# Kernel tuning notes

Measured on AMD Instinct MI355X. Metric: run time of the kernel, lower is better.

The kernel has to match this reference:

```python
import jax, jax.numpy as jnp
import numpy as np

BONE_NUM = 16
THRESH = 0.7


def masked_l2(out, tar, mask):
    # out, tar: [B, C, H, W]; mask: [B, H, W]
    diff_norm = jnp.linalg.norm(out - tar, axis=1)          # [B, H, W]
    masked = jnp.where(mask > THRESH, diff_norm, 0.0)
    B = out.shape[0]
    flat_m = masked.reshape(B, -1)
    flat_d = diff_norm.reshape(B, -1)
    cnt = jnp.sum(flat_m != 0, axis=1)                       # device-side nonzero count
    per_sample = jnp.where(
        cnt > 0,
        flat_m.sum(axis=1) / jnp.maximum(cnt, 1).astype(flat_m.dtype),
        flat_d.mean(axis=1),
    )
    return per_sample.mean()


def pose_nocs_loss(pred_joint_map, pred_joint_score, out_mask, tar_joints):
    # pred_joint_map: [B, bn*3, H, W]; pred_joint_score: [B, bn, H, W]
    # out_mask: [B, H, W]; tar_joints: [B, bn, 3]
    B, _, H, W = pred_joint_map.shape
    bn = BONE_NUM
    jm = pred_joint_map.reshape(B, bn, 3, H, W) * out_mask[:, None, None]
    score = jax.nn.sigmoid(pred_joint_score) * out_mask[:, None]        # [B, bn, H, W]
    denom = score.reshape(B, bn, -1).sum(axis=2)[:, :, None, None] + 1e-5
    score_map = score / denom
    jm = jax.lax.stop_gradient(jm) * score_map[:, :, None]              # [B, bn, 3, H, W]
    pred_joint = jm.reshape(B, bn, 3, -1).sum(axis=3)                   # [B, bn, 3]
    loss = jnp.linalg.norm(pred_joint - tar_joints, axis=2).sum()
    return loss / (B * bn)


def setup_inputs() -> dict:
    key = jax.random.key(0)
    k1, k2, k3 = jax.random.split(key, 3)
    B, H, W = 4, 256, 256
    bn = BONE_NUM
    output = jax.random.normal(k1, (B, 4 + bn * 8 + 2, H, W), dtype=jnp.float32)
    tar_maps = jax.random.uniform(k2, (B, 4 + bn * 6 + 1, H, W), dtype=jnp.float32)
    tar_pose = jax.random.normal(k3, (B, bn, 6), dtype=jnp.float32)
    return {"output": output, "tar_maps": tar_maps, "tar_pose": tar_pose}


def reference(output, tar_maps, tar_pose):
    bn = BONE_NUM
    B = output.shape[0]

    # --- slice predictions ---
    pred_nocs = output[:, 0:3]
    mask_logits = output[:, 3]                                # sigmoid applied below
    pred_loc_map = jax.nn.sigmoid(output[:, 4:4 + bn * 3])
    pred_rot_map = jax.nn.sigmoid(output[:, 4 + bn * 3:4 + bn * 6])
    pred_skin_seg = output[:, 4 + bn * 6:4 + bn * 7 + 2]       # [B, bn+2, H, W]
    pred_joint_score = output[:, 4 + bn * 7 + 2:4 + bn * 8 + 2]  # [B, bn, H, W]

    # --- slice targets ---
    target_nocs = tar_maps[:, 0:3]
    target_mask = tar_maps[:, 3]
    tar_loc_map = jax.nn.sigmoid(tar_maps[:, 4:4 + bn * 3])
    tar_rot_map = jax.nn.sigmoid(tar_maps[:, 4 + bn * 3:4 + bn * 6])
    tar_skin_seg = tar_maps[:, 4 + bn * 6].astype(jnp.int32)   # [B, H, W]
    tar_loc = jax.nn.sigmoid(tar_pose[:, :, 0:3])
    tar_rot = jax.nn.sigmoid(tar_pose[:, :, 3:6])

    # --- BCE mask loss (on sigmoid(mask_logits) vs target_mask), stable form ---
    mask_loss = -jnp.mean(
        target_mask * jax.nn.log_sigmoid(mask_logits)
        + (1.0 - target_mask) * jax.nn.log_sigmoid(-mask_logits)
    )

    # --- masked L2 losses ---
    nocs_loss = masked_l2(pred_nocs, target_nocs, target_mask)
    loc_map_loss = masked_l2(pred_loc_map, tar_loc_map, target_mask)
    rot_map_loss = masked_l2(pred_rot_map, tar_rot_map, target_mask)

    # --- skinning cross entropy ---
    logits = jnp.transpose(pred_skin_seg, (0, 2, 3, 1)).reshape(-1, bn + 2)
    labels = tar_skin_seg.reshape(-1)
    logp = jax.nn.log_softmax(logits, axis=-1)
    skin_loss = -jnp.mean(jnp.take_along_axis(logp, labels[:, None], axis=1))

    # --- pose losses ---
    loc_loss = pose_nocs_loss(pred_loc_map, pred_joint_score, target_mask, tar_loc)
    rot_loss = pose_nocs_loss(pred_rot_map, pred_joint_score, target_mask, tar_rot)

    return jnp.stack([nocs_loss, mask_loss, loc_loss, loc_map_loss,
                      rot_loss, rot_map_loss, skin_loss])
```

## Files before the change

kernel.cpp:

```cpp
#include <hip/hip_runtime.h>
#include <math.h>

#define HW 65536
#define BN 16


__device__ __forceinline__ float fsig(float x) {
    return __builtin_amdgcn_rcpf(1.0f + __expf(-x));
}

__device__ __forceinline__ float wred(float v) {
#pragma unroll
    for (int off = 32; off; off >>= 1) v += __shfl_xor(v, off, 64);
    return v;
}

__global__ __launch_bounds__(256) void mvpm_pix(const float* __restrict__ outp,
                                                const float* __restrict__ tarp,
                                                float* __restrict__ ws) {
    const int b = blockIdx.y;
    const int p = blockIdx.x * 256 + threadIdx.x;
    const float* ob = outp + (size_t)b * 134 * HW;
    const float* tb = tarp + (size_t)b * 101 * HW;
    const int lane = threadIdx.x & 63;
    const int wv = threadIdx.x >> 6;

    const float m = tb[3 * HW + p];
    const bool sel = m > 0.7f;

    const float ml = ob[3 * HW + p];
    const float bce = m * fminf(ml, 0.0f) + (1.0f - m) * fminf(-ml, 0.0f)
                      - __logf(1.0f + __expf(-fabsf(ml)));

    float d0 = ob[0 * HW + p] - tb[0 * HW + p];
    float d1 = ob[1 * HW + p] - tb[1 * HW + p];
    float d2 = ob[2 * HW + p] - tb[2 * HW + p];
    const float dn = sqrtf(d0 * d0 + d1 * d1 + d2 * d2);

    float dsl = 0.0f, dsr = 0.0f;
#pragma unroll 4
    for (int c = 0; c < 48; ++c) {
        float so = fsig(ob[(4 + c) * HW + p]);
        float st = fsig(tb[(4 + c) * HW + p]);
        float d = so - st;
        dsl += d * d;
        float so2 = fsig(ob[(52 + c) * HW + p]);
        float st2 = fsig(tb[(52 + c) * HW + p]);
        float dd = so2 - st2;
        dsr += dd * dd;
    }
    const float dnl = sqrtf(dsl);
    const float dnr = sqrtf(dsr);

    float x[18];
#pragma unroll
    for (int k = 0; k < 18; ++k) x[k] = ob[(100 + k) * HW + p];
    float mx = x[0];
#pragma unroll
    for (int k = 1; k < 18; ++k) mx = fmaxf(mx, x[k]);
    float se = 0.0f;
#pragma unroll
    for (int k = 0; k < 18; ++k) se += __expf(x[k] - mx);
    float lse = mx + __logf(se);
    int lab = (int)tb[100 * HW + p];
    lab = lab < 0 ? 0 : (lab > 17 ? 17 : lab);
    float xl = x[0];
#pragma unroll
    for (int k = 1; k < 18; ++k) xl = (lab == k) ? x[k] : xl;
    const float skin = lse - xl;

    float v[11];
    v[0] = bce;
    v[1] = skin;
    v[2] = sel ? dn : 0.0f;
    v[3] = (sel && dn != 0.0f) ? 1.0f : 0.0f;
    v[4] = dn;
    v[5] = sel ? dnl : 0.0f;
    v[6] = (sel && dnl != 0.0f) ? 1.0f : 0.0f;
    v[7] = dnl;
    v[8] = sel ? dnr : 0.0f;
    v[9] = (sel && dnr != 0.0f) ? 1.0f : 0.0f;
    v[10] = dnr;

#pragma unroll
    for (int off = 32; off; off >>= 1) {
#pragma unroll
        for (int i = 0; i < 11; ++i) v[i] += __shfl_xor(v[i], off, 64);
    }

    __shared__ float red[11][4];
    if (lane == 0) {
#pragma unroll
        for (int i = 0; i < 11; ++i) red[i][wv] = v[i];
    }
    __syncthreads();
    if (threadIdx.x < 11) {
        float s = red[threadIdx.x][0] + red[threadIdx.x][1] +
                  red[threadIdx.x][2] + red[threadIdx.x][3];
        int g = (threadIdx.x < 2) ? threadIdx.x : (2 + b * 9 + (threadIdx.x - 2));
        atomicAdd(&ws[g], s);
    }
}

__global__ __launch_bounds__(256) void mvpm_joint(const float* __restrict__ outp,
                                                  const float* __restrict__ tarp,
                                                  float* __restrict__ ws) {
    const int bj = blockIdx.y;
    const int b = bj >> 4;
    const int j = bj & 15;
    const float* ob = outp + (size_t)b * 134 * HW;
    const float* mp = tarp + (size_t)b * 101 * HW + 3 * HW;
    const float* sp = ob + (118 + j) * HW;
    const float* lp = ob + (4 + 3 * j) * HW;
    const float* rp = ob + (52 + 3 * j) * HW;

    const int base = blockIdx.x * 4096 + threadIdx.x;
    const int lane = threadIdx.x & 63;
    const int wv = threadIdx.x >> 6;

    float S = 0.0f, nl0 = 0.0f, nl1 = 0.0f, nl2 = 0.0f,
          nr0 = 0.0f, nr1 = 0.0f, nr2 = 0.0f;
#pragma unroll 4
    for (int i = 0; i < 16; ++i) {
        const int p = base + i * 256;
        const float m = mp[p];
        const float w = fsig(sp[p]) * m;
        S += w;
        const float wm = w * m;
        nl0 += fsig(lp[p]) * wm;
        nl1 += fsig(lp[HW + p]) * wm;
        nl2 += fsig(lp[2 * HW + p]) * wm;
        nr0 += fsig(rp[p]) * wm;
        nr1 += fsig(rp[HW + p]) * wm;
        nr2 += fsig(rp[2 * HW + p]) * wm;
    }

    float v[7] = {S, nl0, nl1, nl2, nr0, nr1, nr2};
#pragma unroll
    for (int off = 32; off; off >>= 1) {
#pragma unroll
        for (int i = 0; i < 7; ++i) v[i] += __shfl_xor(v[i], off, 64);
    }

    __shared__ float red[7][4];
    if (lane == 0) {
#pragma unroll
        for (int i = 0; i < 7; ++i) red[i][wv] = v[i];
    }
    __syncthreads();
    if (threadIdx.x < 7) {
        float s = red[threadIdx.x][0] + red[threadIdx.x][1] +
                  red[threadIdx.x][2] + red[threadIdx.x][3];
        atomicAdd(&ws[38 + bj * 7 + threadIdx.x], s);
    }
}

__global__ __launch_bounds__(64) void mvpm_fin(const float* __restrict__ ws,
                                               const float* __restrict__ tp,
                                               float* __restrict__ o) {
    const int t = threadIdx.x;
    const int base = 38 + t * 7;

    float S = ws[base] + 1e-5f;
    float ln = 0.0f, rn = 0.0f;
#pragma unroll
    for (int c = 0; c < 3; ++c) {
        float pl = ws[base + 1 + c] / S;
        float tl = 1.0f / (1.0f + expf(-tp[t * 6 + c]));
        ln += (pl - tl) * (pl - tl);
        float pr = ws[base + 4 + c] / S;
        float tr = 1.0f / (1.0f + expf(-tp[t * 6 + 3 + c]));
        rn += (pr - tr) * (pr - tr);
    }
    ln = sqrtf(ln);
    rn = sqrtf(rn);
    float lsum = wred(ln);
    float rsum = wred(rn);

    if (t == 0) {
        float nocs = 0.0f, locm = 0.0f, rotm = 0.0f;
        for (int bb = 0; bb < 4; ++bb) {
            int ba = 2 + bb * 9;
            nocs += (ws[ba + 1] > 0.5f) ? ws[ba + 0] / ws[ba + 1] : ws[ba + 2] * (1.0f / HW);
            locm += (ws[ba + 4] > 0.5f) ? ws[ba + 3] / ws[ba + 4] : ws[ba + 5] * (1.0f / HW);
            rotm += (ws[ba + 7] > 0.5f) ? ws[ba + 6] / ws[ba + 7] : ws[ba + 8] * (1.0f / HW);
        }
        o[0] = nocs * 0.25f;
        o[1] = -ws[0] / (4.0f * HW);
        o[2] = lsum * (1.0f / 64.0f);
        o[3] = locm * 0.25f;
        o[4] = rsum * (1.0f / 64.0f);
        o[5] = rotm * 0.25f;
        o[6] = ws[1] / (4.0f * HW);
    }
}

extern "C" void kernel_launch(void* const* d_in, const int* in_sizes, int n_in,
                              void* d_out, int out_size, void* d_ws, size_t ws_size,
                              hipStream_t stream) {
    const float* outp = (const float*)d_in[0];
    const float* tarp = (const float*)d_in[1];
    const float* tpos = (const float*)d_in[2];
    float* o  = (float*)d_out;
    float* ws = (float*)d_ws;

    hipMemsetAsync(d_ws, 0, 486 * sizeof(float), stream);
    dim3 gA(HW / 256, 4);
    mvpm_pix<<<gA, 256, 0, stream>>>(outp, tarp, ws);
    dim3 gB(16, 64);
    mvpm_joint<<<gB, 256, 0, stream>>>(outp, tarp, ws);
    mvpm_fin<<<1, 64, 0, stream>>>(ws, tpos, o);
}
```

Measured before the change: 294.3 us.

## Fuse joint-weighted pose reduction into per-pixel loss kernel

Merges the separate joint reduction kernel into the per-pixel kernel, so the loc/rot map and score channels are read from memory once instead of twice. Each thread now keeps 112 per-joint partial sums, reduces them across the wave with shuffles, and atomically adds them per block. The skin log-softmax also switches to an online max/sum form. This trades duplicated global reads and a kernel launch for heavy register pressure, many shuffles, and many more atomics per block.

```diff
diff --git a/kernel.cpp b/kernel.cpp
--- a/kernel.cpp
+++ b/kernel.cpp
@@ -15,143 +15,129 @@
     return v;
 }
 
-__global__ __launch_bounds__(256) void mvpm_pix(const float* __restrict__ outp,
-                                                const float* __restrict__ tarp,
-                                                float* __restrict__ ws) {
+__global__ __launch_bounds__(256) void mvpm_fused(const float* __restrict__ outp,
+                                                  const float* __restrict__ tarp,
+                                                  float* __restrict__ ws) {
     const int b = blockIdx.y;
     const int p = blockIdx.x * 256 + threadIdx.x;
-    const float* ob = outp + (size_t)b * 134 * HW;
-    const float* tb = tarp + (size_t)b * 101 * HW;
+    const float* ob = outp + (size_t)b * 134 * HW + p;
+    const float* tb = tarp + (size_t)b * 101 * HW + p;
     const int lane = threadIdx.x & 63;
     const int wv = threadIdx.x >> 6;
 
-    const float m = tb[3 * HW + p];
+    __shared__ float red[123][4];
+
+    const float m = tb[3 * HW];
+    const float mm = m * m;
     const bool sel = m > 0.7f;
 
-    const float ml = ob[3 * HW + p];
+    const float ml = ob[3 * HW];
     const float bce = m * fminf(ml, 0.0f) + (1.0f - m) * fminf(-ml, 0.0f)
                       - __logf(1.0f + __expf(-fabsf(ml)));
 
-    float d0 = ob[0 * HW + p] - tb[0 * HW + p];
-    float d1 = ob[1 * HW + p] - tb[1 * HW + p];
-    float d2 = ob[2 * HW + p] - tb[2 * HW + p];
+    float d0 = ob[0 * HW] - tb[0 * HW];
+    float d1 = ob[1 * HW] - tb[1 * HW];
+    float d2 = ob[2 * HW] - tb[2 * HW];
     const float dn = sqrtf(d0 * d0 + d1 * d1 + d2 * d2);
 
+    float rmax = -1e30f, rsum = 0.0f, xl = 0.0f;
+    const int lab0 = (int)tb[100 * HW];
+    const int lab = lab0 < 0 ? 0 : (lab0 > 17 ? 17 : lab0);
+#pragma unroll
+    for (int k = 0; k < 18; ++k) {
+        float x = ob[(100 + k) * HW];
+        float nm = fmaxf(rmax, x);
+        rsum = rsum * __expf(rmax - nm) + __expf(x - nm);
+        rmax = nm;
+        xl = (lab == k) ? x : xl;
+    }
+    const float skin = rmax + __logf(rsum) - xl;
+
+    {
+        float v[11];
+        v[0] = bce;
+        v[1] = skin;
+        v[2] = sel ? dn : 0.0f;
+        v[3] = (sel && dn != 0.0f) ? 1.0f : 0.0f;
+        v[4] = dn;
+#pragma unroll
+        for (int off = 32; off; off >>= 1) {
+#pragma unroll
+            for (int i = 0; i < 5; ++i) v[i] += __shfl_xor(v[i], off, 64);
+        }
+        if (lane == 0) {
+#pragma unroll
+            for (int i = 0; i < 5; ++i) red[i][wv] = v[i];
+        }
+    }
+
+    float acc[112];
+#pragma unroll
+    for (int i = 0; i < 112; ++i) acc[i] = 0.0f;
+
     float dsl = 0.0f, dsr = 0.0f;
-#pragma unroll 4
-    for (int c = 0; c < 48; ++c) {
-        float so = fsig(ob[(4 + c) * HW + p]);
-        float st = fsig(tb[(4 + c) * HW + p]);
-        float d = so - st;
-        dsl += d * d;
-        float so2 = fsig(ob[(52 + c) * HW + p]);
-        float st2 = fsig(tb[(52 + c) * HW + p]);
-        float dd = so2 - st2;
-        dsr += dd * dd;
+#pragma unroll
+    for (int j = 0; j < BN; ++j) {
+        const float w = fsig(ob[(118 + j) * HW]) * m;
+        acc[j * 7 + 0] = w;
+        const float wm = w * m;
+#pragma unroll
+        for (int k = 0; k < 3; ++k) {
+            const int c = 3 * j + k;
+            float so = fsig(ob[(4 + c) * HW]);
+            float st = fsig(tb[(4 + c) * HW]);
+            float d = so - st;
+            dsl += d * d;
+            acc[j * 7 + 1 + k] = so * wm;
+
+            float so2 = fsig(ob[(52 + c) * HW]);
+            float st2 = fsig(tb[(52 + c) * HW]);
+            float dd = so2 - st2;
+            dsr += dd * dd;
+            acc[j * 7 + 4 + k] = so2 * wm;
+        }
     }
-    const float dnl = sqrtf(dsl);
-    const float dnr = sqrtf(dsr);
 
-    float x[18];
+    {
+        const float dnl = sqrtf(dsl);
+        const float dnr = sqrtf(dsr);
+        float v[6];
+        v[0] = sel ? dnl : 0.0f;
+        v[1] = (sel && dnl != 0.0f) ? 1.0f : 0.0f;
+        v[2] = dnl;
+        v[3] = sel ? dnr : 0.0f;
+        v[4] = (sel && dnr != 0.0f) ? 1.0f : 0.0f;
+        v[5] = dnr;
 #pragma unroll
-    for (int k = 0; k < 18; ++k) x[k] = ob[(100 + k) * HW + p];
-    float mx = x[0];
+        for (int off = 32; off; off >>= 1) {
 #pragma unroll
-    for (int k = 1; k < 18; ++k) mx = fmaxf(mx, x[k]);
-    float se = 0.0f;
+            for (int i = 0; i < 6; ++i) v[i] += __shfl_xor(v[i], off, 64);
+        }
+        if (lane == 0) {
 #pragma unroll
-    for (int k = 0; k < 18; ++k) se += __expf(x[k] - mx);
-    float lse = mx + __logf(se);
-    int lab = (int)tb[100 * HW + p];
-    lab = lab < 0 ? 0 : (lab > 17 ? 17 : lab);
-    float xl = x[0];
-#pragma unroll
-    for (int k = 1; k < 18; ++k) xl = (lab == k) ? x[k] : xl;
-    const float skin = lse - xl;
-
-    float v[11];
-    v[0] = bce;
-    v[1] = skin;
-    v[2] = sel ? dn : 0.0f;
-    v[3] = (sel && dn != 0.0f) ? 1.0f : 0.0f;
-    v[4] = dn;
-    v[5] = sel ? dnl : 0.0f;
-    v[6] = (sel && dnl != 0.0f) ? 1.0f : 0.0f;
-    v[7] = dnl;
-    v[8] = sel ? dnr : 0.0f;
-    v[9] = (sel && dnr != 0.0f) ? 1.0f : 0.0f;
-    v[10] = dnr;
+            for (int i = 0; i < 6; ++i) red[5 + i][wv] = v[i];
+        }
+    }
 
 #pragma unroll
     for (int off = 32; off; off >>= 1) {
 #pragma unroll
-        for (int i = 0; i < 11; ++i) v[i] += __shfl_xor(v[i], off, 64);
+        for (int i = 0; i < 112; ++i) acc[i] += __shfl_xor(acc[i], off, 64);
+    }
+    if (lane == 0) {
+#pragma unroll
+        for (int i = 0; i < 112; ++i) red[11 + i][wv] = acc[i];
     }
 
-    __shared__ float red[11][4];
-    if (lane == 0) {
-#pragma unroll
-        for (int i = 0; i < 11; ++i) red[i][wv] = v[i];
-    }
     __syncthreads();
-    if (threadIdx.x < 11) {
+    if (threadIdx.x < 123) {
         float s = red[threadIdx.x][0] + red[threadIdx.x][1] +
                   red[threadIdx.x][2] + red[threadIdx.x][3];
-        int g = (threadIdx.x < 2) ? threadIdx.x : (2 + b * 9 + (threadIdx.x - 2));
+        int g;
+        if (threadIdx.x < 2)       g = threadIdx.x;
+        else if (threadIdx.x < 11) g = 2 + b * 9 + (threadIdx.x - 2);
+        else                       g = 38 + b * 112 + (threadIdx.x - 11);
         atomicAdd(&ws[g], s);
-    }
-}
-
-__global__ __launch_bounds__(256) void mvpm_joint(const float* __restrict__ outp,
-                                                  const float* __restrict__ tarp,
-                                                  float* __restrict__ ws) {
-    const int bj = blockIdx.y;
-    const int b = bj >> 4;
-    const int j = bj & 15;
-    const float* ob = outp + (size_t)b * 134 * HW;
-    const float* mp = tarp + (size_t)b * 101 * HW + 3 * HW;
-    const float* sp = ob + (118 + j) * HW;
-    const float* lp = ob + (4 + 3 * j) * HW;
-    const float* rp = ob + (52 + 3 * j) * HW;
-
-    const int base = blockIdx.x * 4096 + threadIdx.x;
-    const int lane = threadIdx.x & 63;
-    const int wv = threadIdx.x >> 6;
-
-    float S = 0.0f, nl0 = 0.0f, nl1 = 0.0f, nl2 = 0.0f,
-          nr0 = 0.0f, nr1 = 0.0f, nr2 = 0.0f;
-#pragma unroll 4
-    for (int i = 0; i < 16; ++i) {
-        const int p = base + i * 256;
-        const float m = mp[p];
-        const float w = fsig(sp[p]) * m;
-        S += w;
-        const float wm = w * m;
-        nl0 += fsig(lp[p]) * wm;
-        nl1 += fsig(lp[HW + p]) * wm;
-        nl2 += fsig(lp[2 * HW + p]) * wm;
-        nr0 += fsig(rp[p]) * wm;
-        nr1 += fsig(rp[HW + p]) * wm;
-        nr2 += fsig(rp[2 * HW + p]) * wm;
-    }
-
-    float v[7] = {S, nl0, nl1, nl2, nr0, nr1, nr2};
-#pragma unroll
-    for (int off = 32; off; off >>= 1) {
-#pragma unroll
-        for (int i = 0; i < 7; ++i) v[i] += __shfl_xor(v[i], off, 64);
-    }
-
-    __shared__ float red[7][4];
-    if (lane == 0) {
-#pragma unroll
-        for (int i = 0; i < 7; ++i) red[i][wv] = v[i];
-    }
-    __syncthreads();
-    if (threadIdx.x < 7) {
-        float s = red[threadIdx.x][0] + red[threadIdx.x][1] +
-                  red[threadIdx.x][2] + red[threadIdx.x][3];
-        atomicAdd(&ws[38 + bj * 7 + threadIdx.x], s);
     }
 }
 
@@ -205,9 +191,7 @@
     float* ws = (float*)d_ws;
 
     hipMemsetAsync(d_ws, 0, 486 * sizeof(float), stream);
-    dim3 gA(HW / 256, 4);
-    mvpm_pix<<<gA, 256, 0, stream>>>(outp, tarp, ws);
-    dim3 gB(16, 64);
-    mvpm_joint<<<gB, 256, 0, stream>>>(outp, tarp, ws);
+    dim3 grid(HW / 256, 4);
+    mvpm_fused<<<grid, 256, 0, stream>>>(outp, tarp, ws);
     mvpm_fin<<<1, 64, 0, stream>>>(ws, tpos, o);
 }
```

New measurement: 302.5 us. 2.8% more time.
